# Kernel optimization log

Hardware: AMD Instinct MI355X
Metric: run time of the kernel (lower is better)

## Reference

```python
import jax, jax.numpy as jnp
import numpy as np

N = 100000   # nodes
E = 1200000  # edges
F_IN = 16    # input node features
H = 64       # hidden dim (hard-coded in GinNet)
G = 1024     # graphs in the batch
BN_EPS = 1e-5


def setup_inputs() -> dict:
    key = jax.random.key(0)
    ks = jax.random.split(key, 16)

    def dense(k, shape):
        return (jax.random.normal(k, shape, jnp.float32) * (1.0 / np.sqrt(shape[0]))).astype(jnp.float32)

    x = jax.random.normal(ks[0], (N, F_IN), jnp.float32)
    edge_index = jax.random.randint(ks[1], (2, E), 0, N)
    batch = jnp.sort(jax.random.randint(ks[2], (N,), 0, G))

    inp = {
        'x': x, 'edge_index': edge_index, 'batch': batch,
        # GIN layer 1 (MLP F_IN->H->H, eps, BN affine)
        'W1a': dense(ks[3], (F_IN, H)), 'b1a': jnp.zeros((H,), jnp.float32),
        'W1b': dense(ks[4], (H, H)),    'b1b': jnp.zeros((H,), jnp.float32),
        'eps1': jnp.zeros((), jnp.float32), 'g1': jnp.ones((H,), jnp.float32), 'be1': jnp.zeros((H,), jnp.float32),
        # GIN layer 2
        'W2a': dense(ks[5], (H, H)), 'b2a': jnp.zeros((H,), jnp.float32),
        'W2b': dense(ks[6], (H, H)), 'b2b': jnp.zeros((H,), jnp.float32),
        'eps2': jnp.zeros((), jnp.float32), 'g2': jnp.ones((H,), jnp.float32), 'be2': jnp.zeros((H,), jnp.float32),
        # GIN layer 3
        'W3a': dense(ks[7], (H, H)), 'b3a': jnp.zeros((H,), jnp.float32),
        'W3b': dense(ks[8], (H, H)), 'b3b': jnp.zeros((H,), jnp.float32),
        'eps3': jnp.zeros((), jnp.float32), 'g3': jnp.ones((H,), jnp.float32), 'be3': jnp.zeros((H,), jnp.float32),
        # readout MLP
        'Wf1': dense(ks[9], (H, 10)), 'bf1': jnp.zeros((10,), jnp.float32),
        'Wf2': dense(ks[10], (10, 1)), 'bf2': jnp.zeros((1,), jnp.float32),
    }
    return inp


def _gin_bn(x, edge_index, eps, Wa, ba, Wb, bb, gamma, beta):
    # GINConv: out = MLP((1+eps)*x + sum_{j->i} x_j)
    msgs = x[edge_index[0]]                                      # [E, d] gather
    aggr = jax.ops.segment_sum(msgs, edge_index[1], num_segments=N)  # [N, d] scatter-add
    h = (1.0 + eps) * x + aggr
    h = jnp.maximum(h @ Wa + ba, 0.0) @ Wb + bb                  # Linear-ReLU-Linear
    h = jnp.maximum(h, 0.0)                                      # F.relu after conv
    # BatchNorm1d in training mode: batch statistics (biased var)
    mu = h.mean(axis=0)
    var = h.var(axis=0)
    return gamma * (h - mu) * jax.lax.rsqrt(var + BN_EPS) + beta


def reference(x, edge_index, batch,
              W1a, b1a, W1b, b1b, eps1, g1, be1,
              W2a, b2a, W2b, b2b, eps2, g2, be2,
              W3a, b3a, W3b, b3b, eps3, g3, be3,
              Wf1, bf1, Wf2, bf2):
    h = _gin_bn(x, edge_index, eps1, W1a, b1a, W1b, b1b, g1, be1)
    h = _gin_bn(h, edge_index, eps2, W2a, b2a, W2b, b2b, g2, be2)
    h = _gin_bn(h, edge_index, eps3, W3a, b3a, W3b, b3b, g3, be3)
    # global_mean_pool over graph ids
    sums = jax.ops.segment_sum(h, batch, num_segments=G)                     # [G, H]
    cnt = jax.ops.segment_sum(jnp.ones((N,), jnp.float32), batch, num_segments=G)
    pooled = sums / jnp.maximum(cnt, 1.0)[:, None]
    h = jnp.maximum(pooled @ Wf1 + bf1, 0.0)
    return h @ Wf2 + bf2  # [G, 1]
```

## Files before the change

### kernel.cpp

```cpp
#include <hip/hip_runtime.h>
#include <hip/hip_bf16.h>


#define HD 64
#define NBLK 256
#define BSH 9

typedef unsigned short u16;

__device__ __forceinline__ float bf2f(u16 u) {
    return __uint_as_float(((unsigned int)u) << 16);
}
__device__ __forceinline__ u16 f2bf(float f) {
    unsigned int u = __float_as_uint(f);
    unsigned int r = 0x7FFFu + ((u >> 16) & 1u);
    return (u16)((u + r) >> 16);
}

__global__ void hist_kernel(const int* __restrict__ ei, int* __restrict__ ghist, int E, int C) {
    __shared__ int lh[256];
    int b = blockIdx.x, tid = threadIdx.x;
    lh[tid] = 0;
    __syncthreads();
    int beg = b * C, end = min(beg + C, E);
    for (int i = beg + tid; i < end; i += 256) atomicAdd(&lh[ei[E + i] >> BSH], 1);
    __syncthreads();
    ghist[b * 256 + tid] = lh[tid];
}

__global__ void colscan_kernel(int* __restrict__ ghist, int* __restrict__ total) {
    __shared__ int s[256];
    int k = blockIdx.x, b = threadIdx.x;
    int v = ghist[b * 256 + k];
    s[b] = v;
    __syncthreads();
    for (int off = 1; off < 256; off <<= 1) {
        int u = (b >= off) ? s[b - off] : 0;
        __syncthreads();
        s[b] += u;
        __syncthreads();
    }
    ghist[b * 256 + k] = s[b] - v;
    if (b == 255) total[k] = s[255];
}

__global__ void base_kernel(const int* __restrict__ total, int* __restrict__ bbase, int NBUCK) {
    __shared__ int s[256];
    int t = threadIdx.x;
    int v = (t < NBUCK) ? total[t] : 0;
    s[t] = v;
    __syncthreads();
    for (int off = 1; off < 256; off <<= 1) {
        int u = (t >= off) ? s[t - off] : 0;
        __syncthreads();
        s[t] += u;
        __syncthreads();
    }
    if (t == 0) bbase[0] = 0;
    bbase[t + 1] = s[t];
}

__global__ void scatter_kernel(const int* __restrict__ ei, const int* __restrict__ ghist,
                               const int* __restrict__ bbase, int* __restrict__ bpack,
                               int E, int C) {
    __shared__ int lcur[256];
    int b = blockIdx.x, tid = threadIdx.x;
    lcur[tid] = bbase[tid] + ghist[b * 256 + tid];
    __syncthreads();
    int beg = b * C, end = min(beg + C, E);
    for (int i = beg + tid; i < end; i += 256) {
        int src = ei[i], dst = ei[E + i];
        int pos = atomicAdd(&lcur[dst >> BSH], 1);
        bpack[pos] = src | ((dst & 511) << 17);
    }
}

__global__ void csrbuild_kernel(const int* __restrict__ bpack, const int* __restrict__ bbase,
                                int* __restrict__ row_start, int* __restrict__ csr, int N) {
    __shared__ int h[512], s[512], lc[512];
    int k = blockIdx.x, tid = threadIdx.x;
    int beg = bbase[k], end = bbase[k + 1];
    h[tid] = 0; h[tid + 256] = 0;
    __syncthreads();
    for (int i = beg + tid; i < end; i += 256) atomicAdd(&h[(bpack[i] >> 17) & 511], 1);
    __syncthreads();
    s[tid] = h[tid]; s[tid + 256] = h[tid + 256];
    __syncthreads();
    for (int off = 1; off < 512; off <<= 1) {
        int v0 = (tid >= off) ? s[tid - off] : 0;
        int t1 = tid + 256;
        int v1 = (t1 >= off) ? s[t1 - off] : 0;
        __syncthreads();
        s[tid] += v0; s[t1] += v1;
        __syncthreads();
    }
    int e0 = s[tid] - h[tid], e1 = s[tid + 256] - h[tid + 256];
    lc[tid] = e0; lc[tid + 256] = e1;
    int n0 = (k << BSH) + tid, n1 = (k << BSH) + tid + 256;
    if (n0 < N) row_start[n0] = beg + e0;
    if (n1 < N) row_start[n1] = beg + e1;
    if (k == gridDim.x - 1 && tid == 0) row_start[N] = end;
    __syncthreads();
    for (int i = beg + tid; i < end; i += 256) {
        int v = bpack[i];
        int pos = beg + atomicAdd(&lc[(v >> 17) & 511], 1);
        csr[pos] = v & 0x1FFFF;
    }
}

__global__ void gather64_kernel(const u16* __restrict__ x, const int* __restrict__ rs,
                                const int* __restrict__ csr, float* __restrict__ aggr, int N) {
    int lane = threadIdx.x & 63;
    int l4 = lane & 15;
    int wave = (blockIdx.x * blockDim.x + threadIdx.x) >> 6;
    int n = wave * 4 + (lane >> 4);
    if (n >= N) return;
    int beg = rs[n], end = rs[n + 1];
    const u16* xb = x + (size_t)l4 * 4;
    float a0x = 0, a0y = 0, a0z = 0, a0w = 0;
    float a1x = 0, a1y = 0, a1z = 0, a1w = 0;
    float a2x = 0, a2y = 0, a2z = 0, a2w = 0;
    float a3x = 0, a3y = 0, a3z = 0, a3w = 0;
    for (int base = beg; base < end; base += 16) {
        int cnt = end - base; if (cnt > 16) cnt = 16;
        int e = (l4 < cnt) ? csr[base + l4] : 0;
        int j = 0;
        for (; j + 4 <= cnt; j += 4) {
            int s0 = __shfl(e, j + 0, 16);
            int s1 = __shfl(e, j + 1, 16);
            int s2 = __shfl(e, j + 2, 16);
            int s3 = __shfl(e, j + 3, 16);
            ushort4 u0 = *(const ushort4*)(xb + (size_t)s0 * 64);
            ushort4 u1 = *(const ushort4*)(xb + (size_t)s1 * 64);
            ushort4 u2 = *(const ushort4*)(xb + (size_t)s2 * 64);
            ushort4 u3 = *(const ushort4*)(xb + (size_t)s3 * 64);
            a0x += bf2f(u0.x); a0y += bf2f(u0.y); a0z += bf2f(u0.z); a0w += bf2f(u0.w);
            a1x += bf2f(u1.x); a1y += bf2f(u1.y); a1z += bf2f(u1.z); a1w += bf2f(u1.w);
            a2x += bf2f(u2.x); a2y += bf2f(u2.y); a2z += bf2f(u2.z); a2w += bf2f(u2.w);
            a3x += bf2f(u3.x); a3y += bf2f(u3.y); a3z += bf2f(u3.z); a3w += bf2f(u3.w);
        }
        for (; j < cnt; j++) {
            int s = __shfl(e, j, 16);
            ushort4 u = *(const ushort4*)(xb + (size_t)s * 64);
            a0x += bf2f(u.x); a0y += bf2f(u.y); a0z += bf2f(u.z); a0w += bf2f(u.w);
        }
    }
    float4 o;
    o.x = (a0x + a1x) + (a2x + a3x);
    o.y = (a0y + a1y) + (a2y + a3y);
    o.z = (a0z + a1z) + (a2z + a3z);
    o.w = (a0w + a1w) + (a2w + a3w);
    *reinterpret_cast<float4*>(aggr + (size_t)n * 64 + l4 * 4) = o;
}

__global__ void gather16_kernel(const float* __restrict__ x, const int* __restrict__ rs,
                                const int* __restrict__ csr, float* __restrict__ aggr, int N) {
    int lane = threadIdx.x & 63;
    int l4 = lane & 3;
    int wave = (blockIdx.x * blockDim.x + threadIdx.x) >> 6;
    int n = wave * 16 + (lane >> 2);
    if (n >= N) return;
    int beg = rs[n], end = rs[n + 1];
    const float* xb = x + (size_t)l4 * 4;
    float a0x = 0, a0y = 0, a0z = 0, a0w = 0;
    float a1x = 0, a1y = 0, a1z = 0, a1w = 0;
    float a2x = 0, a2y = 0, a2z = 0, a2w = 0;
    float a3x = 0, a3y = 0, a3z = 0, a3w = 0;
    for (int base = beg; base < end; base += 4) {
        int cnt = end - base; if (cnt > 4) cnt = 4;
        int e = (l4 < cnt) ? csr[base + l4] : 0;
        if (cnt == 4) {
            int s0 = __shfl(e, 0, 4);
            int s1 = __shfl(e, 1, 4);
            int s2 = __shfl(e, 2, 4);
            int s3 = __shfl(e, 3, 4);
            float4 v0 = *(const float4*)(xb + (size_t)s0 * 16);
            float4 v1 = *(const float4*)(xb + (size_t)s1 * 16);
            float4 v2 = *(const float4*)(xb + (size_t)s2 * 16);
            float4 v3 = *(const float4*)(xb + (size_t)s3 * 16);
            a0x += v0.x; a0y += v0.y; a0z += v0.z; a0w += v0.w;
            a1x += v1.x; a1y += v1.y; a1z += v1.z; a1w += v1.w;
            a2x += v2.x; a2y += v2.y; a2z += v2.z; a2w += v2.w;
            a3x += v3.x; a3y += v3.y; a3z += v3.z; a3w += v3.w;
        } else {
            for (int j = 0; j < cnt; j++) {
                int s = __shfl(e, j, 4);
                float4 v = *(const float4*)(xb + (size_t)s * 16);
                a0x += v.x; a0y += v.y; a0z += v.z; a0w += v.w;
            }
        }
    }
    float4 o;
    o.x = (a0x + a1x) + (a2x + a3x);
    o.y = (a0y + a1y) + (a2y + a3y);
    o.z = (a0z + a1z) + (a2z + a3z);
    o.w = (a0w + a1w) + (a2w + a3w);
    *reinterpret_cast<float4*>(aggr + (size_t)n * 16 + l4 * 4) = o;
}

template <int DIN, bool AFF, bool POOL>
__launch_bounds__(256)
__global__ void fused_mlp_kernel(const void* __restrict__ xin_, const float* __restrict__ aggr,
                                 const int* __restrict__ rs, const int* __restrict__ batch,
                                 const float* __restrict__ Wa, const float* __restrict__ ba,
                                 const float* __restrict__ Wb, const float* __restrict__ bb,
                                 const float* __restrict__ epsp,
                                 const float* __restrict__ statsPrev,
                                 const float* __restrict__ gPrev, const float* __restrict__ bePrev,
                                 u16* __restrict__ hout, float* __restrict__ stats,
                                 float* __restrict__ pool, float* __restrict__ cnt, int N) {
    __shared__ float Wa_s[DIN * 64];
    __shared__ float Wb_s[64 * 64];
    __shared__ float zts[64 * 68];
    __shared__ float statS[128];
    __shared__ float degS[64];
    __shared__ float aS[64], cS[64], uS[64];

    const int tid = threadIdx.x;
    const int tc = tid & 15;
    const int tn = tid >> 4;
    const float* xinF = (const float*)xin_;
    const u16*   xinB = (const u16*)xin_;

    const int ITER = 2;
    int blockBase = blockIdx.x * (64 * ITER);

    ushort4 xuP[4]; float4 avP[4];
    float4  xvP, av16P;
    if (DIN == 64) {
#pragma unroll
        for (int i = 0; i < 4; ++i) {
            int node = blockBase + tn * 4 + i;
            xuP[i] = make_ushort4(0, 0, 0, 0);
            avP[i] = make_float4(0, 0, 0, 0);
            if (node < N) {
                xuP[i] = *(const ushort4*)&xinB[(size_t)node * 64 + tc * 4];
                avP[i] = *(const float4*)&aggr[(size_t)node * 64 + tc * 4];
            }
        }
    } else {
        int node = blockBase + tn * 4 + (tc >> 2);
        xvP = make_float4(0, 0, 0, 0);
        av16P = make_float4(0, 0, 0, 0);
        if (node < N) {
            xvP = *(const float4*)&xinF[(size_t)node * 16 + (tc & 3) * 4];
            av16P = *(const float4*)&aggr[(size_t)node * 16 + (tc & 3) * 4];
        }
    }

    if (AFF) {
        if (tid < 64) {
            float invN = 1.0f / (float)N;
            float mu = statsPrev[tid] * invN;
            float var = statsPrev[64 + tid] * invN - mu * mu;
            float inv = rsqrtf(var + 1e-5f);
            float a = gPrev[tid] * inv;
            aS[tid] = a;
            cS[tid] = bePrev[tid] - mu * a;
        }
        __syncthreads();
        for (int i = tid; i < DIN * 64; i += 256) Wa_s[i] = aS[i >> 6] * Wa[i];
        if (tid < 64) {
            float s = 0.0f;
            for (int k = 0; k < 64; k++) s = fmaf(cS[k], Wa[k * 64 + tid], s);
            uS[tid] = s;
        }
    } else {
        for (int i = tid; i < DIN * 64; i += 256) Wa_s[i] = Wa[i];
    }
    for (int i = tid; i < 64 * 64; i += 256) Wb_s[i] = Wb[i];
    if (tid < 128) statS[tid] = 0.0f;
    const float e1 = 1.0f + epsp[0];
    __syncthreads();

    float4 t4;
    t4 = *(const float4*)&ba[tc * 4];
    const float bav[4] = {t4.x, t4.y, t4.z, t4.w};
    t4 = *(const float4*)&bb[tc * 4];
    const float bbv[4] = {t4.x, t4.y, t4.z, t4.w};
    float uv[4] = {0, 0, 0, 0};
    if (AFF) { uv[0] = uS[tc * 4]; uv[1] = uS[tc * 4 + 1]; uv[2] = uS[tc * 4 + 2]; uv[3] = uS[tc * 4 + 3]; }

    float sv[4] = {0, 0, 0, 0}, qv[4] = {0, 0, 0, 0};

    for (int it = 0; it < ITER; ++it) {
        int gbase = blockBase + it * 64;
        float zr[4][4];
        if (DIN == 64) {
#pragma unroll
            for (int i = 0; i < 4; ++i) {
                zr[i][0] = fmaf(e1, bf2f(xuP[i].x), avP[i].x);
                zr[i][1] = fmaf(e1, bf2f(xuP[i].y), avP[i].y);
                zr[i][2] = fmaf(e1, bf2f(xuP[i].z), avP[i].z);
                zr[i][3] = fmaf(e1, bf2f(xuP[i].w), avP[i].w);
            }
        } else {
            zr[0][0] = fmaf(e1, xvP.x, av16P.x);
            zr[0][1] = fmaf(e1, xvP.y, av16P.y);
            zr[0][2] = fmaf(e1, xvP.z, av16P.z);
            zr[0][3] = fmaf(e1, xvP.w, av16P.w);
        }
        if (it + 1 < ITER) {
            int nbase = gbase + 64;
            if (DIN == 64) {
#pragma unroll
                for (int i = 0; i < 4; ++i) {
                    int node = nbase + tn * 4 + i;
                    ushort4 xu = make_ushort4(0, 0, 0, 0);
                    float4 av = make_float4(0, 0, 0, 0);
                    if (node < N) {
                        xu = *(const ushort4*)&xinB[(size_t)node * 64 + tc * 4];
                        av = *(const float4*)&aggr[(size_t)node * 64 + tc * 4];
                    }
                    xuP[i] = xu; avP[i] = av;
                }
            } else {
                int node = nbase + tn * 4 + (tc >> 2);
                float4 xv = make_float4(0, 0, 0, 0), av = make_float4(0, 0, 0, 0);
                if (node < N) {
                    xv = *(const float4*)&xinF[(size_t)node * 16 + (tc & 3) * 4];
                    av = *(const float4*)&aggr[(size_t)node * 16 + (tc & 3) * 4];
                }
                xvP = xv; av16P = av;
            }
        }
        float dg[4];
        if (AFF && tid < 64) {
            int node = gbase + tid;
            degS[tid] = (node < N) ? (float)(rs[node + 1] - rs[node]) : 0.0f;
        }
        __syncthreads();
        if (DIN == 64) {
#pragma unroll
            for (int j = 0; j < 4; ++j) {
                float4 w = {zr[0][j], zr[1][j], zr[2][j], zr[3][j]};
                *(float4*)&zts[(tc * 4 + j) * 68 + tn * 4] = w;
            }
        } else {
#pragma unroll
            for (int j = 0; j < 4; ++j)
                zts[((tc & 3) * 4 + j) * 68 + tn * 4 + (tc >> 2)] = zr[0][j];
        }
        __syncthreads();
        if (AFF) {
#pragma unroll
            for (int i = 0; i < 4; ++i) dg[i] = e1 + degS[tn * 4 + i];
        }
        float ac[4][4];
#pragma unroll
        for (int i = 0; i < 4; ++i)
#pragma unroll
            for (int j = 0; j < 4; ++j)
                ac[i][j] = AFF ? fmaf(dg[i], uv[j], bav[j]) : bav[j];
#pragma unroll 8
        for (int k = 0; k < DIN; ++k) {
            float4 zv = *(const float4*)&zts[k * 68 + tn * 4];
            float4 wv = *(const float4*)&Wa_s[k * 64 + tc * 4];
            const float zf[4] = {zv.x, zv.y, zv.z, zv.w};
            const float wf[4] = {wv.x, wv.y, wv.z, wv.w};
#pragma unroll
            for (int i = 0; i < 4; ++i)
#pragma unroll
                for (int j = 0; j < 4; ++j)
                    ac[i][j] = fmaf(zf[i], wf[j], ac[i][j]);
        }
#pragma unroll
        for (int i = 0; i < 4; ++i)
#pragma unroll
            for (int j = 0; j < 4; ++j)
                ac[i][j] = fmaxf(ac[i][j], 0.0f);
        __syncthreads();
#pragma unroll
        for (int j = 0; j < 4; ++j) {
            float4 w = {ac[0][j], ac[1][j], ac[2][j], ac[3][j]};
            *(float4*)&zts[(tc * 4 + j) * 68 + tn * 4] = w;
        }
        __syncthreads();
        float hc[4][4];
#pragma unroll
        for (int i = 0; i < 4; ++i)
#pragma unroll
            for (int j = 0; j < 4; ++j)
                hc[i][j] = bbv[j];
#pragma unroll 8
        for (int k = 0; k < 64; ++k) {
            float4 tv = *(const float4*)&zts[k * 68 + tn * 4];
            float4 wv = *(const float4*)&Wb_s[k * 64 + tc * 4];
            const float tf[4] = {tv.x, tv.y, tv.z, tv.w};
            const float wf[4] = {wv.x, wv.y, wv.z, wv.w};
#pragma unroll
            for (int i = 0; i < 4; ++i)
#pragma unroll
                for (int j = 0; j < 4; ++j)
                    hc[i][j] = fmaf(tf[i], wf[j], hc[i][j]);
        }
        if (POOL) {
            int curg = -1; float p0 = 0, p1 = 0, p2 = 0, p3 = 0; int run = 0;
#pragma unroll
            for (int i = 0; i < 4; ++i) {
                int node = gbase + tn * 4 + i;
                if (node < N) {
                    float o0 = fmaxf(hc[i][0], 0.0f), o1 = fmaxf(hc[i][1], 0.0f);
                    float o2 = fmaxf(hc[i][2], 0.0f), o3 = fmaxf(hc[i][3], 0.0f);
                    sv[0] += o0; sv[1] += o1; sv[2] += o2; sv[3] += o3;
                    qv[0] += o0 * o0; qv[1] += o1 * o1; qv[2] += o2 * o2; qv[3] += o3 * o3;
                    int gid = batch[node];
                    if (gid != curg) {
                        if (curg >= 0) {
                            unsafeAtomicAdd(&pool[(size_t)curg * 64 + tc * 4 + 0], p0);
                            unsafeAtomicAdd(&pool[(size_t)curg * 64 + tc * 4 + 1], p1);
                            unsafeAtomicAdd(&pool[(size_t)curg * 64 + tc * 4 + 2], p2);
                            unsafeAtomicAdd(&pool[(size_t)curg * 64 + tc * 4 + 3], p3);
                            if (tc == 0) unsafeAtomicAdd(&cnt[curg], (float)run);
                        }
                        curg = gid; p0 = p1 = p2 = p3 = 0.0f; run = 0;
                    }
                    p0 += o0; p1 += o1; p2 += o2; p3 += o3; run++;
                }
            }
            if (curg >= 0) {
                unsafeAtomicAdd(&pool[(size_t)curg * 64 + tc * 4 + 0], p0);
                unsafeAtomicAdd(&pool[(size_t)curg * 64 + tc * 4 + 1], p1);
                unsafeAtomicAdd(&pool[(size_t)curg * 64 + tc * 4 + 2], p2);
                unsafeAtomicAdd(&pool[(size_t)curg * 64 + tc * 4 + 3], p3);
                if (tc == 0) unsafeAtomicAdd(&cnt[curg], (float)run);
            }
        } else {
#pragma unroll
            for (int i = 0; i < 4; ++i) {
                int node = gbase + tn * 4 + i;
                if (node < N) {
                    float o0 = fmaxf(hc[i][0], 0.0f), o1 = fmaxf(hc[i][1], 0.0f);
                    float o2 = fmaxf(hc[i][2], 0.0f), o3 = fmaxf(hc[i][3], 0.0f);
                    ushort4 ob = {f2bf(o0), f2bf(o1), f2bf(o2), f2bf(o3)};
                    *(ushort4*)&hout[(size_t)node * 64 + tc * 4] = ob;
                    sv[0] += o0; sv[1] += o1; sv[2] += o2; sv[3] += o3;
                    qv[0] += o0 * o0; qv[1] += o1 * o1; qv[2] += o2 * o2; qv[3] += o3 * o3;
                }
            }
        }
    }
#pragma unroll
    for (int off = 16; off < 64; off <<= 1) {
#pragma unroll
        for (int j = 0; j < 4; ++j) {
            sv[j] += __shfl_xor(sv[j], off);
            qv[j] += __shfl_xor(qv[j], off);
        }
    }
    if ((tid & 63) < 16) {
#pragma unroll
        for (int j = 0; j < 4; ++j) {
            atomicAdd(&statS[tc * 4 + j], sv[j]);
            atomicAdd(&statS[64 + tc * 4 + j], qv[j]);
        }
    }
    __syncthreads();
    if (tid < 128) unsafeAtomicAdd(&stats[tid], statS[tid]);
}

__global__ void readout_kernel(const float* __restrict__ pool, const float* __restrict__ cnt,
                               const float* __restrict__ stats, const float* __restrict__ g3,
                               const float* __restrict__ be3,
                               const float* __restrict__ Wf1, const float* __restrict__ bf1,
                               const float* __restrict__ Wf2, const float* __restrict__ bf2,
                               float* __restrict__ out, int N) {
    int gb = blockIdx.x;
    int t = threadIdx.x;
    float invN = 1.0f / (float)N;
    float mu = stats[t] * invN;
    float var = stats[64 + t] * invN - mu * mu;
    float inv = rsqrtf(var + 1e-5f);
    float a = g3[t] * inv;
    float c = be3[t] - mu * a;
    float cn = cnt[gb];
    float p = (cn > 0.0f) ? (a * (pool[(size_t)gb * 64 + t] / cn) + c) : 0.0f;
    float o = 0.0f;
#pragma unroll
    for (int j = 0; j < 10; j++) {
        float part = p * Wf1[t * 10 + j];
#pragma unroll
        for (int off = 32; off > 0; off >>= 1) part += __shfl_down(part, off);
        float z = fmaxf(part + bf1[j], 0.0f);
        o = fmaf(z, Wf2[j], o);
    }
    if (t == 0) out[gb] = o + bf2[0];
}

extern "C" void kernel_launch(void* const* d_in, const int* in_sizes, int n_in,
                              void* d_out, int out_size, void* d_ws, size_t ws_size,
                              hipStream_t stream) {
    const float* x      = (const float*)d_in[0];
    const int*   ei     = (const int*)d_in[1];
    const int*   batch  = (const int*)d_in[2];
    const float* W1a = (const float*)d_in[3];  const float* b1a = (const float*)d_in[4];
    const float* W1b = (const float*)d_in[5];  const float* b1b = (const float*)d_in[6];
    const float* e1  = (const float*)d_in[7];  const float* g1  = (const float*)d_in[8];
    const float* be1 = (const float*)d_in[9];
    const float* W2a = (const float*)d_in[10]; const float* b2a = (const float*)d_in[11];
    const float* W2b = (const float*)d_in[12]; const float* b2b = (const float*)d_in[13];
    const float* e2  = (const float*)d_in[14]; const float* g2  = (const float*)d_in[15];
    const float* be2 = (const float*)d_in[16];
    const float* W3a = (const float*)d_in[17]; const float* b3a = (const float*)d_in[18];
    const float* W3b = (const float*)d_in[19]; const float* b3b = (const float*)d_in[20];
    const float* e3  = (const float*)d_in[21]; const float* g3  = (const float*)d_in[22];
    const float* be3 = (const float*)d_in[23];
    const float* Wf1 = (const float*)d_in[24]; const float* bf1 = (const float*)d_in[25];
    const float* Wf2 = (const float*)d_in[26]; const float* bf2 = (const float*)d_in[27];

    const int N = in_sizes[2];
    const int E = in_sizes[1] / 2;
    const int G = out_size;
    const int NBUCK = (N + 511) >> BSH;
    const int C = (E + NBLK - 1) / NBLK;

    int* csr       = (int*)d_ws;
    int* row_start = csr + E;
    int* bpack     = row_start + N + 64;
    int* ghist     = bpack + E;
    int* total     = ghist + NBLK * 256;
    int* bbase     = total + 256;
    float* stats   = (float*)(bbase + 272);
    float* pool    = stats + 384;
    float* cnt     = pool + (size_t)G * HD;
    float* aggr    = cnt + G;
    size_t NH = (size_t)N * HD;
    u16* hA        = (u16*)(aggr + NH);
    u16* hB        = hA + NH;

    const int TB = 256;
    int fusedGrid = (N + 127) / 128;
    size_t zeroBytes = (size_t)(384 + (size_t)G * HD + G) * sizeof(float);

    hipMemsetAsync(stats, 0, zeroBytes, stream);
    hist_kernel<<<NBLK, 256, 0, stream>>>(ei, ghist, E, C);
    colscan_kernel<<<NBUCK, 256, 0, stream>>>(ghist, total);
    base_kernel<<<1, 256, 0, stream>>>(total, bbase, NBUCK);
    scatter_kernel<<<NBLK, 256, 0, stream>>>(ei, ghist, bbase, bpack, E, C);
    csrbuild_kernel<<<NBUCK, 256, 0, stream>>>(bpack, bbase, row_start, csr, N);

    gather16_kernel<<<((N + 15) / 16 * 64 + TB - 1) / TB, TB, 0, stream>>>(x, row_start, csr, aggr, N);
    fused_mlp_kernel<16, false, false><<<fusedGrid, TB, 0, stream>>>(
        x, aggr, row_start, batch, W1a, b1a, W1b, b1b, e1,
        nullptr, nullptr, nullptr, hA, stats, nullptr, nullptr, N);

    gather64_kernel<<<((N + 3) / 4 * 64 + TB - 1) / TB, TB, 0, stream>>>(hA, row_start, csr, aggr, N);
    fused_mlp_kernel<64, true, false><<<fusedGrid, TB, 0, stream>>>(
        hA, aggr, row_start, batch, W2a, b2a, W2b, b2b, e2,
        stats, g1, be1, hB, stats + 128, nullptr, nullptr, N);

    gather64_kernel<<<((N + 3) / 4 * 64 + TB - 1) / TB, TB, 0, stream>>>(hB, row_start, csr, aggr, N);
    fused_mlp_kernel<64, true, true><<<fusedGrid, TB, 0, stream>>>(
        hB, aggr, row_start, batch, W3a, b3a, W3b, b3b, e3,
        stats + 128, g2, be2, hA , stats + 256, pool, cnt, N);

    readout_kernel<<<G, 64, 0, stream>>>(pool, cnt, stats + 256, g3, be3,
                                         Wf1, bf1, Wf2, bf2, (float*)d_out, N);
}
```

Before: 406.5 us.

## Shrink fused MLP LDS footprint, one tile per block, replicate BN stat accumulators

The fused MLP kernel now processes one 64-node tile per block instead of two, and shares a single 64x64 LDS weight buffer between both layers. The second weight matrix is held in registers and copied into LDS after the first GEMM finishes. This cuts LDS use per block to raise occupancy, and doubles the block count. BN statistics are spread over 8 replicated accumulators selected by block index to reduce atomic contention, and consumers sum the replicas. The cost is more per-block weight loading and an extra register array.

```diff
diff --git a/kernel.cpp b/kernel.cpp
--- a/kernel.cpp
+++ b/kernel.cpp
@@ -5,15 +5,17 @@
 #define HD 64
 #define NBLK 256
 #define BSH 9
+#define SREP 8
 
 typedef unsigned short u16;
+typedef unsigned int u32;
 
 __device__ __forceinline__ float bf2f(u16 u) {
-    return __uint_as_float(((unsigned int)u) << 16);
+    return __uint_as_float(((u32)u) << 16);
 }
 __device__ __forceinline__ u16 f2bf(float f) {
-    unsigned int u = __float_as_uint(f);
-    unsigned int r = 0x7FFFu + ((u >> 16) & 1u);
+    u32 u = __float_as_uint(f);
+    u32 r = 0x7FFFu + ((u >> 16) & 1u);
     return (u16)((u + r) >> 16);
 }
 
@@ -209,8 +211,7 @@
                                  const float* __restrict__ gPrev, const float* __restrict__ bePrev,
                                  u16* __restrict__ hout, float* __restrict__ stats,
                                  float* __restrict__ pool, float* __restrict__ cnt, int N) {
-    __shared__ float Wa_s[DIN * 64];
-    __shared__ float Wb_s[64 * 64];
+    __shared__ float W_s[64 * 64];
     __shared__ float zts[64 * 68];
     __shared__ float statS[128];
     __shared__ float degS[64];
@@ -222,8 +223,7 @@
     const float* xinF = (const float*)xin_;
     const u16*   xinB = (const u16*)xin_;
 
-    const int ITER = 2;
-    int blockBase = blockIdx.x * (64 * ITER);
+    int blockBase = blockIdx.x * 64;
 
     ushort4 xuP[4]; float4 avP[4];
     float4  xvP, av16P;
@@ -247,196 +247,174 @@
             av16P = *(const float4*)&aggr[(size_t)node * 16 + (tc & 3) * 4];
         }
     }
+    float wbR[16];
+#pragma unroll
+    for (int i = 0; i < 16; ++i) wbR[i] = Wb[tid + i * 256];
 
     if (AFF) {
         if (tid < 64) {
             float invN = 1.0f / (float)N;
-            float mu = statsPrev[tid] * invN;
-            float var = statsPrev[64 + tid] * invN - mu * mu;
+            float s0 = 0, s1 = 0;
+#pragma unroll
+            for (int r = 0; r < SREP; ++r) {
+                s0 += statsPrev[r * 128 + tid];
+                s1 += statsPrev[r * 128 + 64 + tid];
+            }
+            float mu = s0 * invN;
+            float var = s1 * invN - mu * mu;
             float inv = rsqrtf(var + 1e-5f);
             float a = gPrev[tid] * inv;
             aS[tid] = a;
             cS[tid] = bePrev[tid] - mu * a;
         }
         __syncthreads();
-        for (int i = tid; i < DIN * 64; i += 256) Wa_s[i] = aS[i >> 6] * Wa[i];
+        for (int i = tid; i < DIN * 64; i += 256) W_s[i] = aS[i >> 6] * Wa[i];
         if (tid < 64) {
             float s = 0.0f;
             for (int k = 0; k < 64; k++) s = fmaf(cS[k], Wa[k * 64 + tid], s);
             uS[tid] = s;
         }
     } else {
-        for (int i = tid; i < DIN * 64; i += 256) Wa_s[i] = Wa[i];
-    }
-    for (int i = tid; i < 64 * 64; i += 256) Wb_s[i] = Wb[i];
+        for (int i = tid; i < DIN * 64; i += 256) W_s[i] = Wa[i];
+    }
     if (tid < 128) statS[tid] = 0.0f;
     const float e1 = 1.0f + epsp[0];
-    __syncthreads();
+    if (AFF && tid < 64) {
+        int node = blockBase + tid;
+        degS[tid] = (node < N) ? (float)(rs[node + 1] - rs[node]) : 0.0f;
+    }
 
     float4 t4;
     t4 = *(const float4*)&ba[tc * 4];
     const float bav[4] = {t4.x, t4.y, t4.z, t4.w};
     t4 = *(const float4*)&bb[tc * 4];
     const float bbv[4] = {t4.x, t4.y, t4.z, t4.w};
+
+    float sv[4] = {0, 0, 0, 0}, qv[4] = {0, 0, 0, 0};
+
+    float zr[4][4];
+    if (DIN == 64) {
+#pragma unroll
+        for (int i = 0; i < 4; ++i) {
+            zr[i][0] = fmaf(e1, bf2f(xuP[i].x), avP[i].x);
+            zr[i][1] = fmaf(e1, bf2f(xuP[i].y), avP[i].y);
+            zr[i][2] = fmaf(e1, bf2f(xuP[i].z), avP[i].z);
+            zr[i][3] = fmaf(e1, bf2f(xuP[i].w), avP[i].w);
+        }
+#pragma unroll
+        for (int j = 0; j < 4; ++j) {
+            float4 w = {zr[0][j], zr[1][j], zr[2][j], zr[3][j]};
+            *(float4*)&zts[(tc * 4 + j) * 68 + tn * 4] = w;
+        }
+    } else {
+        zr[0][0] = fmaf(e1, xvP.x, av16P.x);
+        zr[0][1] = fmaf(e1, xvP.y, av16P.y);
+        zr[0][2] = fmaf(e1, xvP.z, av16P.z);
+        zr[0][3] = fmaf(e1, xvP.w, av16P.w);
+#pragma unroll
+        for (int j = 0; j < 4; ++j)
+            zts[((tc & 3) * 4 + j) * 68 + tn * 4 + (tc >> 2)] = zr[0][j];
+    }
+    __syncthreads();
     float uv[4] = {0, 0, 0, 0};
     if (AFF) { uv[0] = uS[tc * 4]; uv[1] = uS[tc * 4 + 1]; uv[2] = uS[tc * 4 + 2]; uv[3] = uS[tc * 4 + 3]; }
-
-    float sv[4] = {0, 0, 0, 0}, qv[4] = {0, 0, 0, 0};
-
-    for (int it = 0; it < ITER; ++it) {
-        int gbase = blockBase + it * 64;
-        float zr[4][4];
-        if (DIN == 64) {
-#pragma unroll
-            for (int i = 0; i < 4; ++i) {
-                zr[i][0] = fmaf(e1, bf2f(xuP[i].x), avP[i].x);
-                zr[i][1] = fmaf(e1, bf2f(xuP[i].y), avP[i].y);
-                zr[i][2] = fmaf(e1, bf2f(xuP[i].z), avP[i].z);
-                zr[i][3] = fmaf(e1, bf2f(xuP[i].w), avP[i].w);
+    float dg[4];
+    if (AFF) {
+#pragma unroll
+        for (int i = 0; i < 4; ++i) dg[i] = e1 + degS[tn * 4 + i];
+    }
+    float ac[4][4];
+#pragma unroll
+    for (int i = 0; i < 4; ++i)
+#pragma unroll
+        for (int j = 0; j < 4; ++j)
+            ac[i][j] = AFF ? fmaf(dg[i], uv[j], bav[j]) : bav[j];
+#pragma unroll 8
+    for (int k = 0; k < DIN; ++k) {
+        float4 zv = *(const float4*)&zts[k * 68 + tn * 4];
+        float4 wv = *(const float4*)&W_s[k * 64 + tc * 4];
+        const float zf[4] = {zv.x, zv.y, zv.z, zv.w};
+        const float wf[4] = {wv.x, wv.y, wv.z, wv.w};
+#pragma unroll
+        for (int i = 0; i < 4; ++i)
+#pragma unroll
+            for (int j = 0; j < 4; ++j)
+                ac[i][j] = fmaf(zf[i], wf[j], ac[i][j]);
+    }
+#pragma unroll
+    for (int i = 0; i < 4; ++i)
+#pragma unroll
+        for (int j = 0; j < 4; ++j)
+            ac[i][j] = fmaxf(ac[i][j], 0.0f);
+    __syncthreads();
+#pragma unroll
+    for (int j = 0; j < 4; ++j) {
+        float4 w = {ac[0][j], ac[1][j], ac[2][j], ac[3][j]};
+        *(float4*)&zts[(tc * 4 + j) * 68 + tn * 4] = w;
+    }
+#pragma unroll
+    for (int i = 0; i < 16; ++i) W_s[tid + i * 256] = wbR[i];
+    __syncthreads();
+    float hc[4][4];
+#pragma unroll
+    for (int i = 0; i < 4; ++i)
+#pragma unroll
+        for (int j = 0; j < 4; ++j)
+            hc[i][j] = bbv[j];
+#pragma unroll 8
+    for (int k = 0; k < 64; ++k) {
+        float4 tv = *(const float4*)&zts[k * 68 + tn * 4];
+        float4 wv = *(const float4*)&W_s[k * 64 + tc * 4];
+        const float tf[4] = {tv.x, tv.y, tv.z, tv.w};
+        const float wf[4] = {wv.x, wv.y, wv.z, wv.w};
+#pragma unroll
+        for (int i = 0; i < 4; ++i)
+#pragma unroll
+            for (int j = 0; j < 4; ++j)
+                hc[i][j] = fmaf(tf[i], wf[j], hc[i][j]);
+    }
+    if (POOL) {
+        int curg = -1; float p0 = 0, p1 = 0, p2 = 0, p3 = 0; int run = 0;
+#pragma unroll
+        for (int i = 0; i < 4; ++i) {
+            int node = blockBase + tn * 4 + i;
+            if (node < N) {
+                float o0 = fmaxf(hc[i][0], 0.0f), o1 = fmaxf(hc[i][1], 0.0f);
+                float o2 = fmaxf(hc[i][2], 0.0f), o3 = fmaxf(hc[i][3], 0.0f);
+                sv[0] += o0; sv[1] += o1; sv[2] += o2; sv[3] += o3;
+                qv[0] += o0 * o0; qv[1] += o1 * o1; qv[2] += o2 * o2; qv[3] += o3 * o3;
+                int gid = batch[node];
+                if (gid != curg) {
+                    if (curg >= 0) {
+                        unsafeAtomicAdd(&pool[(size_t)curg * 64 + tc * 4 + 0], p0);
+                        unsafeAtomicAdd(&pool[(size_t)curg * 64 + tc * 4 + 1], p1);
+                        unsafeAtomicAdd(&pool[(size_t)curg * 64 + tc * 4 + 2], p2);
+                        unsafeAtomicAdd(&pool[(size_t)curg * 64 + tc * 4 + 3], p3);
+                        if (tc == 0) unsafeAtomicAdd(&cnt[curg], (float)run);
+                    }
+                    curg = gid; p0 = p1 = p2 = p3 = 0.0f; run = 0;
+                }
+                p0 += o0; p1 += o1; p2 += o2; p3 += o3; run++;
             }
-        } else {
-            zr[0][0] = fmaf(e1, xvP.x, av16P.x);
-            zr[0][1] = fmaf(e1, xvP.y, av16P.y);
-            zr[0][2] = fmaf(e1, xvP.z, av16P.z);
-            zr[0][3] = fmaf(e1, xvP.w, av16P.w);
-        }
-        if (it + 1 < ITER) {
-            int nbase = gbase + 64;
-            if (DIN == 64) {
-#pragma unroll
-                for (int i = 0; i < 4; ++i) {
-                    int node = nbase + tn * 4 + i;
-                    ushort4 xu = make_ushort4(0, 0, 0, 0);
-                    float4 av = make_float4(0, 0, 0, 0);
-                    if (node < N) {
-                        xu = *(const ushort4*)&xinB[(size_t)node * 64 + tc * 4];
-                        av = *(const float4*)&aggr[(size_t)node * 64 + tc * 4];
-                    }
-                    xuP[i] = xu; avP[i] = av;
-                }
-            } else {
-                int node = nbase + tn * 4 + (tc >> 2);
-                float4 xv = make_float4(0, 0, 0, 0), av = make_float4(0, 0, 0, 0);
-                if (node < N) {
-                    xv = *(const float4*)&xinF[(size_t)node * 16 + (tc & 3) * 4];
-                    av = *(const float4*)&aggr[(size_t)node * 16 + (tc & 3) * 4];
-                }
-                xvP = xv; av16P = av;
-            }
-        }
-        float dg[4];
-        if (AFF && tid < 64) {
-            int node = gbase + tid;
-            degS[tid] = (node < N) ? (float)(rs[node + 1] - rs[node]) : 0.0f;
-        }
-        __syncthreads();
-        if (DIN == 64) {
-#pragma unroll
-            for (int j = 0; j < 4; ++j) {
-                float4 w = {zr[0][j], zr[1][j], zr[2][j], zr[3][j]};
-                *(float4*)&zts[(tc * 4 + j) * 68 + tn * 4] = w;
-            }
-        } else {
-#pragma unroll
-            for (int j = 0; j < 4; ++j)
-                zts[((tc & 3) * 4 + j) * 68 + tn * 4 + (tc >> 2)] = zr[0][j];
-        }
-        __syncthreads();
-        if (AFF) {
-#pragma unroll
-            for (int i = 0; i < 4; ++i) dg[i] = e1 + degS[tn * 4 + i];
-        }
-        float ac[4][4];
-#pragma unroll
-        for (int i = 0; i < 4; ++i)
-#pragma unroll
-            for (int j = 0; j < 4; ++j)
-                ac[i][j] = AFF ? fmaf(dg[i], uv[j], bav[j]) : bav[j];
-#pragma unroll 8
-        for (int k = 0; k < DIN; ++k) {
-            float4 zv = *(const float4*)&zts[k * 68 + tn * 4];
-            float4 wv = *(const float4*)&Wa_s[k * 64 + tc * 4];
-            const float zf[4] = {zv.x, zv.y, zv.z, zv.w};
-            const float wf[4] = {wv.x, wv.y, wv.z, wv.w};
-#pragma unroll
-            for (int i = 0; i < 4; ++i)
-#pragma unroll
-                for (int j = 0; j < 4; ++j)
-                    ac[i][j] = fmaf(zf[i], wf[j], ac[i][j]);
-        }
-#pragma unroll
-        for (int i = 0; i < 4; ++i)
-#pragma unroll
-            for (int j = 0; j < 4; ++j)
-                ac[i][j] = fmaxf(ac[i][j], 0.0f);
-        __syncthreads();
-#pragma unroll
-        for (int j = 0; j < 4; ++j) {
-            float4 w = {ac[0][j], ac[1][j], ac[2][j], ac[3][j]};
-            *(float4*)&zts[(tc * 4 + j) * 68 + tn * 4] = w;
-        }
-        __syncthreads();
-        float hc[4][4];
-#pragma unroll
-        for (int i = 0; i < 4; ++i)
-#pragma unroll
-            for (int j = 0; j < 4; ++j)
-                hc[i][j] = bbv[j];
-#pragma unroll 8
-        for (int k = 0; k < 64; ++k) {
-            float4 tv = *(const float4*)&zts[k * 68 + tn * 4];
-            float4 wv = *(const float4*)&Wb_s[k * 64 + tc * 4];
-            const float tf[4] = {tv.x, tv.y, tv.z, tv.w};
-            const float wf[4] = {wv.x, wv.y, wv.z, wv.w};
-#pragma unroll
-            for (int i = 0; i < 4; ++i)
-#pragma unroll
-                for (int j = 0; j < 4; ++j)
-                    hc[i][j] = fmaf(tf[i], wf[j], hc[i][j]);
-        }
-        if (POOL) {
-            int curg = -1; float p0 = 0, p1 = 0, p2 = 0, p3 = 0; int run = 0;
-#pragma unroll
-            for (int i = 0; i < 4; ++i) {
-                int node = gbase + tn * 4 + i;
-                if (node < N) {
-                    float o0 = fmaxf(hc[i][0], 0.0f), o1 = fmaxf(hc[i][1], 0.0f);
-                    float o2 = fmaxf(hc[i][2], 0.0f), o3 = fmaxf(hc[i][3], 0.0f);
-                    sv[0] += o0; sv[1] += o1; sv[2] += o2; sv[3] += o3;
-                    qv[0] += o0 * o0; qv[1] += o1 * o1; qv[2] += o2 * o2; qv[3] += o3 * o3;
-                    int gid = batch[node];
-                    if (gid != curg) {
-                        if (curg >= 0) {
-                            unsafeAtomicAdd(&pool[(size_t)curg * 64 + tc * 4 + 0], p0);
-                            unsafeAtomicAdd(&pool[(size_t)curg * 64 + tc * 4 + 1], p1);
-                            unsafeAtomicAdd(&pool[(size_t)curg * 64 + tc * 4 + 2], p2);
-                            unsafeAtomicAdd(&pool[(size_t)curg * 64 + tc * 4 + 3], p3);
-                            if (tc == 0) unsafeAtomicAdd(&cnt[curg], (float)run);
-                        }
-                        curg = gid; p0 = p1 = p2 = p3 = 0.0f; run = 0;
-                    }
-                    p0 += o0; p1 += o1; p2 += o2; p3 += o3; run++;
-                }
-            }
-            if (curg >= 0) {
-                unsafeAtomicAdd(&pool[(size_t)curg * 64 + tc * 4 + 0], p0);
-                unsafeAtomicAdd(&pool[(size_t)curg * 64 + tc * 4 + 1], p1);
-                unsafeAtomicAdd(&pool[(size_t)curg * 64 + tc * 4 + 2], p2);
-                unsafeAtomicAdd(&pool[(size_t)curg * 64 + tc * 4 + 3], p3);
-                if (tc == 0) unsafeAtomicAdd(&cnt[curg], (float)run);
-            }
-        } else {
-#pragma unroll
-            for (int i = 0; i < 4; ++i) {
-                int node = gbase + tn * 4 + i;
-                if (node < N) {
-                    float o0 = fmaxf(hc[i][0], 0.0f), o1 = fmaxf(hc[i][1], 0.0f);
-                    float o2 = fmaxf(hc[i][2], 0.0f), o3 = fmaxf(hc[i][3], 0.0f);
-                    ushort4 ob = {f2bf(o0), f2bf(o1), f2bf(o2), f2bf(o3)};
-                    *(ushort4*)&hout[(size_t)node * 64 + tc * 4] = ob;
-                    sv[0] += o0; sv[1] += o1; sv[2] += o2; sv[3] += o3;
-                    qv[0] += o0 * o0; qv[1] += o1 * o1; qv[2] += o2 * o2; qv[3] += o3 * o3;
-                }
+        }
+        if (curg >= 0) {
+            unsafeAtomicAdd(&pool[(size_t)curg * 64 + tc * 4 + 0], p0);
+            unsafeAtomicAdd(&pool[(size_t)curg * 64 + tc * 4 + 1], p1);
+            unsafeAtomicAdd(&pool[(size_t)curg * 64 + tc * 4 + 2], p2);
+            unsafeAtomicAdd(&pool[(size_t)curg * 64 + tc * 4 + 3], p3);
+            if (tc == 0) unsafeAtomicAdd(&cnt[curg], (float)run);
+        }
+    } else {
+#pragma unroll
+        for (int i = 0; i < 4; ++i) {
+            int node = blockBase + tn * 4 + i;
+            if (node < N) {
+                float o0 = fmaxf(hc[i][0], 0.0f), o1 = fmaxf(hc[i][1], 0.0f);
+                float o2 = fmaxf(hc[i][2], 0.0f), o3 = fmaxf(hc[i][3], 0.0f);
+                ushort4 ob = {f2bf(o0), f2bf(o1), f2bf(o2), f2bf(o3)};
+                *(ushort4*)&hout[(size_t)node * 64 + tc * 4] = ob;
+                sv[0] += o0; sv[1] += o1; sv[2] += o2; sv[3] += o3;
+                qv[0] += o0 * o0; qv[1] += o1 * o1; qv[2] += o2 * o2; qv[3] += o3 * o3;
             }
         }
     }
@@ -456,7 +434,7 @@
         }
     }
     __syncthreads();
-    if (tid < 128) unsafeAtomicAdd(&stats[tid], statS[tid]);
+    if (tid < 128) unsafeAtomicAdd(&stats[(blockIdx.x & (SREP - 1)) * 128 + tid], statS[tid]);
 }
 
 __global__ void readout_kernel(const float* __restrict__ pool, const float* __restrict__ cnt,
@@ -468,8 +446,14 @@
     int gb = blockIdx.x;
     int t = threadIdx.x;
     float invN = 1.0f / (float)N;
-    float mu = stats[t] * invN;
-    float var = stats[64 + t] * invN - mu * mu;
+    float s0 = 0, s1 = 0;
+#pragma unroll
+    for (int r = 0; r < SREP; ++r) {
+        s0 += stats[r * 128 + t];
+        s1 += stats[r * 128 + 64 + t];
+    }
+    float mu = s0 * invN;
+    float var = s1 * invN - mu * mu;
     float inv = rsqrtf(var + 1e-5f);
     float a = g3[t] * inv;
     float c = be3[t] - mu * a;
@@ -521,7 +505,7 @@
     int* total     = ghist + NBLK * 256;
     int* bbase     = total + 256;
     float* stats   = (float*)(bbase + 272);
-    float* pool    = stats + 384;
+    float* pool    = stats + 3 * SREP * 128;
     float* cnt     = pool + (size_t)G * HD;
     float* aggr    = cnt + G;
     size_t NH = (size_t)N * HD;
@@ -529,8 +513,8 @@
     u16* hB        = hA + NH;
 
     const int TB = 256;
-    int fusedGrid = (N + 127) / 128;
-    size_t zeroBytes = (size_t)(384 + (size_t)G * HD + G) * sizeof(float);
+    int fusedGrid = (N + 63) / 64;
+    size_t zeroBytes = (size_t)(3 * SREP * 128 + (size_t)G * HD + G) * sizeof(float);
 
     hipMemsetAsync(stats, 0, zeroBytes, stream);
     hist_kernel<<<NBLK, 256, 0, stream>>>(ei, ghist, E, C);
@@ -547,13 +531,13 @@
     gather64_kernel<<<((N + 3) / 4 * 64 + TB - 1) / TB, TB, 0, stream>>>(hA, row_start, csr, aggr, N);
     fused_mlp_kernel<64, true, false><<<fusedGrid, TB, 0, stream>>>(
         hA, aggr, row_start, batch, W2a, b2a, W2b, b2b, e2,
-        stats, g1, be1, hB, stats + 128, nullptr, nullptr, N);
+        stats, g1, be1, hB, stats + SREP * 128, nullptr, nullptr, N);
 
     gather64_kernel<<<((N + 3) / 4 * 64 + TB - 1) / TB, TB, 0, stream>>>(hB, row_start, csr, aggr, N);
     fused_mlp_kernel<64, true, true><<<fusedGrid, TB, 0, stream>>>(
         hB, aggr, row_start, batch, W3a, b3a, W3b, b3b, e3,
-        stats + 128, g2, be2, hA , stats + 256, pool, cnt, N);
-
-    readout_kernel<<<G, 64, 0, stream>>>(pool, cnt, stats + 256, g3, be3,
+        stats + SREP * 128, g2, be2, hA , stats + 2 * SREP * 128, pool, cnt, N);
+
+    readout_kernel<<<G, 64, 0, stream>>>(pool, cnt, stats + 2 * SREP * 128, g3, be3,
                                          Wf1, bf1, Wf2, bf2, (float*)d_out, N);
 }
```

Result: faster. 383.3 us (-5.7%).
